# Kernel optimization log

Hardware: AMD Instinct MI355X
Metric: run time of the kernel (lower is better)

## Reference

```python
import jax, jax.numpy as jnp
import numpy as np

EPS = 1e-06

def _quantize_weights(W):
    # absmean ternary quantization: sign(W/gamma) * clamp(round(|W/gamma|), max=1)
    gamma = jnp.mean(jnp.abs(W)) + EPS
    Ws = W / gamma
    return jnp.sign(Ws) * jnp.minimum(jnp.round(jnp.abs(Ws)), 1.0)

def setup_inputs() -> dict:
    key = jax.random.key(0)
    kx, kw = jax.random.split(key)
    x = jax.random.normal(kx, (4, 2048, 4096), dtype=jnp.float32)
    weight = jax.random.normal(kw, (16384, 4096), dtype=jnp.float32)
    return {"x": x, "weight": weight}

def reference(x, weight):
    xs = jnp.sign(x)                       # binarized activations in {-1,0,1}
    Wq = _quantize_weights(weight)          # ternary weights in {-1,0,1}
    # F.linear(x, W) == x @ W.T ; [b, s, in] x [out, in] -> [b, s, out]
    return jnp.einsum('bsi,oi->bso', xs, Wq)
```

## Files before the change

### kernel.cpp

```cpp
#include <hip/hip_runtime.h>
#include <hip/hip_bf16.h>
#include <cstdint>

constexpr int Mx = 8192;
constexpr int Kx = 4096;
constexpr int Nx = 16384;
constexpr long W_ELEMS = (long)Nx * Kx;
constexpr long X_ELEMS = (long)Mx * Kx;
constexpr int KB = Kx / 2;

typedef int v4i __attribute__((ext_vector_type(4)));
typedef int v8i __attribute__((ext_vector_type(8)));
typedef float v16f __attribute__((ext_vector_type(16)));

#define GLOBAL_AS(p) ((const __attribute__((address_space(1))) void*)(p))
#define LDS_AS(p)    ((__attribute__((address_space(3))) void*)(p))

template <int P> struct IC { static constexpr int value = P; };

__global__ __launch_bounds__(256) void absum_kernel(const float4* __restrict__ W4,
                                                    double* __restrict__ partials) {
    int t = threadIdx.x;
    long base = (long)blockIdx.x * 8192;
    double s = 0.0;
#pragma unroll 4
    for (int i = 0; i < 32; ++i) {
        float4 v = W4[base + (long)i * 256 + t];
        s += (double)fabsf(v.x) + (double)fabsf(v.y) +
             (double)fabsf(v.z) + (double)fabsf(v.w);
    }
    __shared__ double sm[256];
    sm[t] = s;
    __syncthreads();
    for (int off = 128; off > 0; off >>= 1) {
        if (t < off) sm[t] += sm[t + off];
        __syncthreads();
    }
    if (t == 0) partials[blockIdx.x] = sm[0];
}

__global__ __launch_bounds__(256) void finalize_kernel(const double* __restrict__ partials,
                                                       float* __restrict__ thr) {
    int t = threadIdx.x;
    double s = 0.0;
#pragma unroll
    for (int i = 0; i < 8; ++i) s += partials[(long)i * 256 + t];
    __shared__ double sm[256];
    sm[t] = s;
    __syncthreads();
    for (int off = 128; off > 0; off >>= 1) {
        if (t < off) sm[t] += sm[t + off];
        __syncthreads();
    }
    if (t == 0) {
        double gamma = sm[0] / (double)W_ELEMS + 1e-6;
        *thr = (float)(0.5 * gamma);
    }
}

__device__ __forceinline__ uint32_t enc_t(float v, float thr) {
    return (fabsf(v) > thr) ? ((v > 0.f) ? 0x2u : 0xAu) : 0x0u;
}

__device__ __forceinline__ uint32_t pack8(float4 a, float4 b, float thr) {
    return enc_t(a.x, thr)        | (enc_t(a.y, thr) << 4)  |
          (enc_t(a.z, thr) << 8)  | (enc_t(a.w, thr) << 12) |
          (enc_t(b.x, thr) << 16) | (enc_t(b.y, thr) << 20) |
          (enc_t(b.z, thr) << 24) | (enc_t(b.w, thr) << 28);
}

__global__ __launch_bounds__(256) void quantw_kernel(const float4* __restrict__ W4,
                                                     uint4* __restrict__ out,
                                                     const float* __restrict__ thrp) {
    float thr = *thrp;
    long gt = (long)blockIdx.x * 256 + threadIdx.x;
    uint32_t d0 = pack8(W4[gt * 8 + 0], W4[gt * 8 + 1], thr);
    uint32_t d1 = pack8(W4[gt * 8 + 2], W4[gt * 8 + 3], thr);
    uint32_t d2 = pack8(W4[gt * 8 + 4], W4[gt * 8 + 5], thr);
    uint32_t d3 = pack8(W4[gt * 8 + 6], W4[gt * 8 + 7], thr);
    out[gt] = make_uint4(d0, d1, d2, d3);
}

__global__ __launch_bounds__(256) void quantx_kernel(const float4* __restrict__ X4,
                                                     uint4* __restrict__ out) {
    long gt = (long)blockIdx.x * 256 + threadIdx.x;
    uint32_t d0 = pack8(X4[gt * 8 + 0], X4[gt * 8 + 1], 0.f);
    uint32_t d1 = pack8(X4[gt * 8 + 2], X4[gt * 8 + 3], 0.f);
    uint32_t d2 = pack8(X4[gt * 8 + 4], X4[gt * 8 + 5], 0.f);
    uint32_t d3 = pack8(X4[gt * 8 + 6], X4[gt * 8 + 7], 0.f);
    out[gt] = make_uint4(d0, d1, d2, d3);
}

__global__ __launch_bounds__(512) void gemm_fp4(const uint8_t* __restrict__ A,
                                                const uint8_t* __restrict__ B,
                                                float* __restrict__ C) {
    __shared__ __align__(16) uint8_t smem[8 * 16384];

    const int t = threadIdx.x;
    const int l = t & 63;
    const int wid = t >> 6;
    const int wm = wid >> 2;
    const int wn = wid & 3;
    const int lr = l & 31;
    const int lh = l >> 5;

    int wg = blockIdx.x;
    int sw = (wg & 7) * 256 + (wg >> 3);
    int bm = sw & 31;
    int bn = sw >> 5;
    const long m0 = (long)bm * 256;
    const long n0 = (long)bn * 256;

    const int r0s = t >> 2;
    const int cb0 = (((t & 3) ^ ((r0s >> 1) & 3)) << 4);
    const int voff0 = r0s * KB + cb0;
    const int voff1 = voff0 + 128 * KB;
    const uint8_t* Abase = A + m0 * (long)KB;
    const uint8_t* Bbase = B + n0 * (long)KB;
    const int lo0 = t * 16, lo1 = t * 16 + 8192;

    auto swz = [](int r, int c) {
        return r * 64 + ((c ^ ((r >> 1) & 3)) << 4);
    };
    int offA[2][4], offB[2][2];
#pragma unroll
    for (int h = 0; h < 2; ++h) {
#pragma unroll
        for (int mt = 0; mt < 4; ++mt)
            offA[h][mt] = swz(wm * 128 + mt * 32 + lr, h * 2 + lh);
#pragma unroll
        for (int nt = 0; nt < 2; ++nt)
            offB[h][nt] = swz(wn * 64 + nt * 32 + lr, h * 2 + lh);
    }

    v16f acc[4][2] = {};

#pragma unroll
    for (int j = 0; j < 5; ++j) {
        int tj = j >> 1, slot = j;
        const uint8_t* s = (j & 1) ? Bbase : Abase;
        __builtin_amdgcn_global_load_lds(GLOBAL_AS(s + tj * 64 + voff0), LDS_AS(smem + slot * 16384 + lo0), 16, 0, 0);
        __builtin_amdgcn_global_load_lds(GLOBAL_AS(s + tj * 64 + voff1), LDS_AS(smem + slot * 16384 + lo1), 16, 0, 0);
    }
    asm volatile("s_waitcnt vmcnt(6)" ::: "memory");
    asm volatile("s_barrier" ::: "memory");

#pragma unroll 2
    for (int tau = 0; tau < 32; ++tau) {
        auto phase = [&](auto hc) {
            constexpr int h = decltype(hc)::value;
            const int sA = (2 * tau) & 7;
            const int sB = (2 * tau + 1) & 7;
            v8i ar8[4], br8[2];
#pragma unroll
            for (int mt = 0; mt < 4; ++mt) {
                v4i v = *(const v4i*)(smem + sA * 16384 + offA[h][mt]);
                ar8[mt] = __builtin_shufflevector(v, v, 0, 1, 2, 3, -1, -1, -1, -1);
            }
#pragma unroll
            for (int nt = 0; nt < 2; ++nt) {
                v4i v = *(const v4i*)(smem + sB * 16384 + offB[h][nt]);
                br8[nt] = __builtin_shufflevector(v, v, 0, 1, 2, 3, -1, -1, -1, -1);
            }
            {
                int j = 2 * tau + h + 5;
                if (j < 64) {
                    int tj = j >> 1, slot = j & 7;
                    const uint8_t* s = (j & 1) ? Bbase : Abase;
                    __builtin_amdgcn_global_load_lds(GLOBAL_AS(s + tj * 64 + voff0), LDS_AS(smem + slot * 16384 + lo0), 16, 0, 0);
                    __builtin_amdgcn_global_load_lds(GLOBAL_AS(s + tj * 64 + voff1), LDS_AS(smem + slot * 16384 + lo1), 16, 0, 0);
                }
            }
            asm volatile("s_barrier" ::: "memory");
            __builtin_amdgcn_s_setprio(1);
#pragma unroll
            for (int mt = 0; mt < 4; ++mt)
#pragma unroll
                for (int nt = 0; nt < 2; ++nt)
                    acc[mt][nt] = __builtin_amdgcn_mfma_scale_f32_32x32x64_f8f6f4(
                        ar8[mt], br8[nt], acc[mt][nt], 4, 4, 0, 0x7F7F7F7F, 0, 0x7F7F7F7F);
            __builtin_amdgcn_s_setprio(0);
            if constexpr (h == 1) {
                if (tau <= 28)      asm volatile("s_waitcnt vmcnt(6)" ::: "memory");
                else if (tau == 29) asm volatile("s_waitcnt vmcnt(4)" ::: "memory");
                else if (tau == 30) asm volatile("s_waitcnt vmcnt(0)" ::: "memory");
            }
            asm volatile("s_barrier" ::: "memory");
        };
        phase(IC<0>{});
        phase(IC<1>{});
    }

#pragma unroll
    for (int mt = 0; mt < 4; ++mt) {
        long rbase = m0 + wm * 128 + mt * 32 + 4 * lh;
#pragma unroll
        for (int nt = 0; nt < 2; ++nt) {
            long gcol = n0 + wn * 64 + nt * 32 + lr;
#pragma unroll
            for (int r = 0; r < 16; ++r) {
                long grow = rbase + (r & 3) + 8 * (r >> 2);
                C[grow * Nx + gcol] = acc[mt][nt][r];
            }
        }
    }
}

extern "C" void kernel_launch(void* const* d_in, const int* in_sizes, int n_in,
                              void* d_out, int out_size, void* d_ws, size_t ws_size,
                              hipStream_t stream) {
    const float* x = (const float*)d_in[0];
    const float* weight = (const float*)d_in[1];
    float* out = (float*)d_out;

    uint8_t* xq = (uint8_t*)d_ws;
    uint8_t* wq = xq + X_ELEMS / 2;
    double* partials = (double*)((char*)d_ws + X_ELEMS / 2 + W_ELEMS / 2);
    float* thr = (float*)((char*)d_ws + X_ELEMS / 2 + W_ELEMS / 2 + 2048 * sizeof(double));

    absum_kernel<<<2048, 256, 0, stream>>>((const float4*)weight, partials);
    finalize_kernel<<<1, 256, 0, stream>>>(partials, thr);
    quantw_kernel<<<8192, 256, 0, stream>>>((const float4*)weight, (uint4*)wq, thr);
    quantx_kernel<<<4096, 256, 0, stream>>>((const float4*)x, (uint4*)xq);
    gemm_fp4<<<2048, 512, 0, stream>>>(xq, wq, out);
}
```

Measured before the change: 573.8 us.

## Restructure GEMM main loop with one barrier per k-step and interleaved LDS reads

Reorganizes the fp4 GEMM pipeline so each k-tile loads A and B together (4 async loads per step, prefetch depth 3 tiles) and only one barrier is issued per k-step instead of two per half-step. The second half's LDS reads are placed after the first half's MFMAs so they can overlap with matrix work, and the loop is unrolled 4. The aim is less synchronization overhead and better latency hiding. The risks are higher register pressure and a tighter LDS slot reuse window.

```diff
diff --git a/kernel.cpp b/kernel.cpp
--- a/kernel.cpp
+++ b/kernel.cpp
@@ -15,8 +15,6 @@
 
 #define GLOBAL_AS(p) ((const __attribute__((address_space(1))) void*)(p))
 #define LDS_AS(p)    ((__attribute__((address_space(3))) void*)(p))
-
-template <int P> struct IC { static constexpr int value = P; };
 
 __global__ __launch_bounds__(256) void absum_kernel(const float4* __restrict__ W4,
                                                     double* __restrict__ partials) {
@@ -136,59 +134,81 @@
     v16f acc[4][2] = {};
 
 #pragma unroll
-    for (int j = 0; j < 5; ++j) {
-        int tj = j >> 1, slot = j;
-        const uint8_t* s = (j & 1) ? Bbase : Abase;
-        __builtin_amdgcn_global_load_lds(GLOBAL_AS(s + tj * 64 + voff0), LDS_AS(smem + slot * 16384 + lo0), 16, 0, 0);
-        __builtin_amdgcn_global_load_lds(GLOBAL_AS(s + tj * 64 + voff1), LDS_AS(smem + slot * 16384 + lo1), 16, 0, 0);
-    }
-    asm volatile("s_waitcnt vmcnt(6)" ::: "memory");
+    for (int pt = 0; pt < 3; ++pt) {
+        long koff = (long)pt * 64;
+        __builtin_amdgcn_global_load_lds(GLOBAL_AS(Abase + koff + voff0), LDS_AS(smem + (2 * pt) * 16384 + lo0), 16, 0, 0);
+        __builtin_amdgcn_global_load_lds(GLOBAL_AS(Abase + koff + voff1), LDS_AS(smem + (2 * pt) * 16384 + lo1), 16, 0, 0);
+        __builtin_amdgcn_global_load_lds(GLOBAL_AS(Bbase + koff + voff0), LDS_AS(smem + (2 * pt + 1) * 16384 + lo0), 16, 0, 0);
+        __builtin_amdgcn_global_load_lds(GLOBAL_AS(Bbase + koff + voff1), LDS_AS(smem + (2 * pt + 1) * 16384 + lo1), 16, 0, 0);
+    }
+    asm volatile("s_waitcnt vmcnt(8)" ::: "memory");
     asm volatile("s_barrier" ::: "memory");
 
-#pragma unroll 2
+#pragma unroll 4
     for (int tau = 0; tau < 32; ++tau) {
-        auto phase = [&](auto hc) {
-            constexpr int h = decltype(hc)::value;
-            const int sA = (2 * tau) & 7;
-            const int sB = (2 * tau + 1) & 7;
-            v8i ar8[4], br8[2];
+        const int sA = (2 * tau) & 7;
+        const int sB = sA + 1;
+
+        v4i a0[4], b0[2];
+#pragma unroll
+        for (int mt = 0; mt < 4; ++mt)
+            a0[mt] = *(const v4i*)(smem + sA * 16384 + offA[0][mt]);
+#pragma unroll
+        for (int nt = 0; nt < 2; ++nt)
+            b0[nt] = *(const v4i*)(smem + sB * 16384 + offB[0][nt]);
+
+        if (tau <= 28) {
+            const int slA2 = (2 * tau + 6) & 7;
+            const int slB2 = (2 * tau + 7) & 7;
+            const long koff = (long)(tau + 3) * 64;
+            __builtin_amdgcn_global_load_lds(GLOBAL_AS(Abase + koff + voff0), LDS_AS(smem + slA2 * 16384 + lo0), 16, 0, 0);
+            __builtin_amdgcn_global_load_lds(GLOBAL_AS(Abase + koff + voff1), LDS_AS(smem + slA2 * 16384 + lo1), 16, 0, 0);
+            __builtin_amdgcn_global_load_lds(GLOBAL_AS(Bbase + koff + voff0), LDS_AS(smem + slB2 * 16384 + lo0), 16, 0, 0);
+            __builtin_amdgcn_global_load_lds(GLOBAL_AS(Bbase + koff + voff1), LDS_AS(smem + slB2 * 16384 + lo1), 16, 0, 0);
+        }
+
+        {
+            v8i b80 = __builtin_shufflevector(b0[0], b0[0], 0, 1, 2, 3, -1, -1, -1, -1);
+            v8i b81 = __builtin_shufflevector(b0[1], b0[1], 0, 1, 2, 3, -1, -1, -1, -1);
+            __builtin_amdgcn_s_setprio(1);
 #pragma unroll
             for (int mt = 0; mt < 4; ++mt) {
-                v4i v = *(const v4i*)(smem + sA * 16384 + offA[h][mt]);
-                ar8[mt] = __builtin_shufflevector(v, v, 0, 1, 2, 3, -1, -1, -1, -1);
+                v8i a8 = __builtin_shufflevector(a0[mt], a0[mt], 0, 1, 2, 3, -1, -1, -1, -1);
+                acc[mt][0] = __builtin_amdgcn_mfma_scale_f32_32x32x64_f8f6f4(
+                    a8, b80, acc[mt][0], 4, 4, 0, 0x7F7F7F7F, 0, 0x7F7F7F7F);
+                acc[mt][1] = __builtin_amdgcn_mfma_scale_f32_32x32x64_f8f6f4(
+                    a8, b81, acc[mt][1], 4, 4, 0, 0x7F7F7F7F, 0, 0x7F7F7F7F);
             }
-#pragma unroll
-            for (int nt = 0; nt < 2; ++nt) {
-                v4i v = *(const v4i*)(smem + sB * 16384 + offB[h][nt]);
-                br8[nt] = __builtin_shufflevector(v, v, 0, 1, 2, 3, -1, -1, -1, -1);
+            __builtin_amdgcn_s_setprio(0);
+        }
+
+        v4i a1[4], b1[2];
+#pragma unroll
+        for (int mt = 0; mt < 4; ++mt)
+            a1[mt] = *(const v4i*)(smem + sA * 16384 + offA[1][mt]);
+#pragma unroll
+        for (int nt = 0; nt < 2; ++nt)
+            b1[nt] = *(const v4i*)(smem + sB * 16384 + offB[1][nt]);
+
+        {
+            v8i b80 = __builtin_shufflevector(b1[0], b1[0], 0, 1, 2, 3, -1, -1, -1, -1);
+            v8i b81 = __builtin_shufflevector(b1[1], b1[1], 0, 1, 2, 3, -1, -1, -1, -1);
+            __builtin_amdgcn_s_setprio(1);
+#pragma unroll
+            for (int mt = 0; mt < 4; ++mt) {
+                v8i a8 = __builtin_shufflevector(a1[mt], a1[mt], 0, 1, 2, 3, -1, -1, -1, -1);
+                acc[mt][0] = __builtin_amdgcn_mfma_scale_f32_32x32x64_f8f6f4(
+                    a8, b80, acc[mt][0], 4, 4, 0, 0x7F7F7F7F, 0, 0x7F7F7F7F);
+                acc[mt][1] = __builtin_amdgcn_mfma_scale_f32_32x32x64_f8f6f4(
+                    a8, b81, acc[mt][1], 4, 4, 0, 0x7F7F7F7F, 0, 0x7F7F7F7F);
             }
-            {
-                int j = 2 * tau + h + 5;
-                if (j < 64) {
-                    int tj = j >> 1, slot = j & 7;
-                    const uint8_t* s = (j & 1) ? Bbase : Abase;
-                    __builtin_amdgcn_global_load_lds(GLOBAL_AS(s + tj * 64 + voff0), LDS_AS(smem + slot * 16384 + lo0), 16, 0, 0);
-                    __builtin_amdgcn_global_load_lds(GLOBAL_AS(s + tj * 64 + voff1), LDS_AS(smem + slot * 16384 + lo1), 16, 0, 0);
-                }
-            }
-            asm volatile("s_barrier" ::: "memory");
-            __builtin_amdgcn_s_setprio(1);
-#pragma unroll
-            for (int mt = 0; mt < 4; ++mt)
-#pragma unroll
-                for (int nt = 0; nt < 2; ++nt)
-                    acc[mt][nt] = __builtin_amdgcn_mfma_scale_f32_32x32x64_f8f6f4(
-                        ar8[mt], br8[nt], acc[mt][nt], 4, 4, 0, 0x7F7F7F7F, 0, 0x7F7F7F7F);
             __builtin_amdgcn_s_setprio(0);
-            if constexpr (h == 1) {
-                if (tau <= 28)      asm volatile("s_waitcnt vmcnt(6)" ::: "memory");
-                else if (tau == 29) asm volatile("s_waitcnt vmcnt(4)" ::: "memory");
-                else if (tau == 30) asm volatile("s_waitcnt vmcnt(0)" ::: "memory");
-            }
-            asm volatile("s_barrier" ::: "memory");
-        };
-        phase(IC<0>{});
-        phase(IC<1>{});
+        }
+
+        if (tau <= 28)      asm volatile("s_waitcnt vmcnt(8)" ::: "memory");
+        else if (tau == 29) asm volatile("s_waitcnt vmcnt(4)" ::: "memory");
+        else if (tau == 30) asm volatile("s_waitcnt vmcnt(0)" ::: "memory");
+        asm volatile("s_barrier" ::: "memory");
     }
 
 #pragma unroll
```

Result: slower. 1.678 ms (+192.4%).
